# Kernel optimization log

Hardware: AMD Instinct MI355X
Metric: run time of the kernel (lower is better)

Reference implementation:

```python
import jax, jax.numpy as jnp
import numpy as np

N = 100000      # nodes
E = 1600000     # edges (avg degree 16)
IN_F, HID, OUT_F, NC = 384, 128, 64, 2
EPS = 1e-5
NEG_SLOPE = 0.01


def _layernorm(x, g, b):
    m = jnp.mean(x, axis=-1, keepdims=True)
    v = jnp.var(x, axis=-1, keepdims=True)
    return (x - m) * jax.lax.rsqrt(v + EPS) * g + b


def _graph_conv(x, edge_index, edge_weight, w_rel, b_rel, w_root):
    # PyG GraphConv: lin_rel(scatter_add(w_e * x[src] -> dst)) + lin_root(x)
    src, dst = edge_index[0], edge_index[1]
    msg = x[src] * edge_weight[:, None]                      # [E, C]
    agg = jax.ops.segment_sum(msg, dst, num_segments=x.shape[0])  # [N, C]
    return agg @ w_rel.T + b_rel + x @ w_root.T


def _xavier(key, shape):
    fan_in, fan_out = shape[1], shape[0]
    lim = float(np.sqrt(6.0 / (fan_in + fan_out)))
    return jax.random.uniform(key, shape, jnp.float32, -lim, lim)


def setup_inputs() -> dict:
    key = jax.random.key(0)
    ks = jax.random.split(key, 10)
    x = jax.random.normal(ks[0], (N, IN_F), jnp.float32)
    edge_index = jax.random.randint(ks[1], (2, E), 0, N, jnp.int64)
    edge_attr = jax.random.uniform(ks[2], (E,), jnp.float32)
    return {
        "x": x,
        "edge_index": edge_index,
        "edge_attr": edge_attr,
        "ln1_g": jnp.ones((IN_F,), jnp.float32),
        "ln1_b": jnp.zeros((IN_F,), jnp.float32),
        "fc1_w": _xavier(ks[3], (HID, IN_F)),
        "fc1_b": jnp.zeros((HID,), jnp.float32),
        "c1_wrel": _xavier(ks[4], (HID, HID)),
        "c1_brel": jnp.zeros((HID,), jnp.float32),
        "c1_wroot": _xavier(ks[5], (HID, HID)),
        "c2_wrel": _xavier(ks[6], (OUT_F, HID)),
        "c2_brel": jnp.zeros((OUT_F,), jnp.float32),
        "c2_wroot": _xavier(ks[7], (OUT_F, HID)),
        "ln2_g": jnp.ones((OUT_F,), jnp.float32),
        "ln2_b": jnp.zeros((OUT_F,), jnp.float32),
        "fc2_w": _xavier(ks[8], (NC, OUT_F)),
        "fc2_b": jnp.zeros((NC,), jnp.float32),
    }


def reference(x, edge_index, edge_attr,
              ln1_g, ln1_b, fc1_w, fc1_b,
              c1_wrel, c1_brel, c1_wroot,
              c2_wrel, c2_brel, c2_wroot,
              ln2_g, ln2_b, fc2_w, fc2_b):
    h = _layernorm(x, ln1_g, ln1_b) @ fc1_w.T + fc1_b          # [N, HID]
    h = _graph_conv(h, edge_index, edge_attr, c1_wrel, c1_brel, c1_wroot)
    h = jax.nn.leaky_relu(h, NEG_SLOPE)
    h = _graph_conv(h, edge_index, edge_attr, c2_wrel, c2_brel, c2_wroot)
    h = jax.nn.leaky_relu(h, NEG_SLOPE)                        # [N, OUT_F]
    out = _layernorm(h, ln2_g, ln2_b) @ fc2_w.T + fc2_b        # [N, NC]
    return out
```

## Files before the change

kernel.cpp:

```cpp
#include <hip/hip_runtime.h>
#include <hip/hip_bf16.h>

#define N_IN_F 384
#define N_HID  128
#define N_OUT  64

typedef unsigned short ushort_t;
typedef __attribute__((ext_vector_type(8))) short short8v;
typedef __attribute__((ext_vector_type(4))) float floatx4;

union U8 { uint4 v; unsigned short u[8]; };

__device__ __forceinline__ float bfu2f(unsigned short s){
    union { unsigned i; float f; } c; c.i = ((unsigned)s) << 16; return c.f;
}
__device__ __forceinline__ unsigned short f2bfu(float f){
    __hip_bfloat16 h = __float2bfloat16(f);
    union { __hip_bfloat16 h; unsigned short u; } c; c.h = h; return c.u;
}

__device__ __forceinline__ float loadS(const void* p, size_t i, int fm){
    return fm ? bfu2f(((const unsigned short*)p)[i]) : ((const float*)p)[i];
}

__global__ void k_detect_all(const int* __restrict__ ei, const unsigned* __restrict__ xw,
                             int* __restrict__ modep){
    int lane = threadIdx.x & 63;
    int zi = 0;
    if (lane < 32) zi = ei[2*lane + 1];
    int cnt = 0;
    #pragma unroll
    for (int q = 0; q < 8; q++){
        unsigned w = xw[lane*8 + q];
        unsigned elo = (w >> 7) & 0xff;
        cnt += (elo >= 118 && elo <= 134) ? 1 : 0;
    }
    #pragma unroll
    for (int m = 32; m; m >>= 1){ zi |= __shfl_xor(zi, m, 64); cnt += __shfl_xor(cnt, m, 64); }
    if (lane == 0 && blockIdx.x == 0){
        modep[0] = (zi == 0) ? 1 : 0;
        modep[1] = (cnt >= 256) ? 1 : 0;
    }
}

__device__ __forceinline__ int edge_src(const int* ei, int e, int i, int mode){
    return mode ? ei[2*(size_t)i] : ei[i];
}
__device__ __forceinline__ int edge_dst(const int* ei, int e, int i, int mode){
    return mode ? ei[2*(size_t)e + 2*(size_t)i] : ei[(size_t)e + i];
}

__global__ void k_hist(const int* __restrict__ ei, int e, int n, const int* __restrict__ modep,
                       int* __restrict__ deg, unsigned* __restrict__ rel){
    int i = blockIdx.x * 256 + threadIdx.x;
    if (i >= e) return;
    int mode = modep[0];
    int d = edge_dst(ei, e, i, mode);
    if ((unsigned)d >= (unsigned)n) return;
    rel[i] = (unsigned)atomicAdd(&deg[d], 1);
}

__global__ __launch_bounds__(1024) void k_blksum(
    const int* __restrict__ deg, int n, int* __restrict__ part)
{
    __shared__ int s[1024];
    int i = blockIdx.x * 1024 + threadIdx.x;
    s[threadIdx.x] = (i < n) ? deg[i] : 0;
    __syncthreads();
    for (int off = 512; off; off >>= 1){
        if (threadIdx.x < off) s[threadIdx.x] += s[threadIdx.x + off];
        __syncthreads();
    }
    if (threadIdx.x == 0) part[blockIdx.x] = s[0];
}

__global__ __launch_bounds__(128) void k_scanpart(
    int* __restrict__ part, int nb, int* __restrict__ rowoff, int n)
{
    __shared__ int s[128];
    int t = threadIdx.x;
    if (nb <= 128){
        int v = (t < nb) ? part[t] : 0;
        s[t] = v; __syncthreads();
        #pragma unroll
        for (int off = 1; off < 128; off <<= 1){
            int tmp = (t >= off) ? s[t - off] : 0;
            __syncthreads();
            s[t] += tmp;
            __syncthreads();
        }
        if (t < nb) part[t] = s[t] - v;
        if (t == 127) rowoff[n] = s[127];
    } else if (t == 0){
        int run = 0;
        for (int b = 0; b < nb; b++){ int tt = part[b]; part[b] = run; run += tt; }
        rowoff[n] = run;
    }
}

__global__ __launch_bounds__(1024) void k_scanblk(
    int* __restrict__ deg, const int* __restrict__ part, int n, int* __restrict__ rowoff)
{
    __shared__ int s[1024];
    int t = threadIdx.x;
    int i = blockIdx.x * 1024 + t;
    int v = (i < n) ? deg[i] : 0;
    s[t] = v; __syncthreads();
    for (int off = 1; off < 1024; off <<= 1){
        int tmp = (t >= off) ? s[t - off] : 0;
        __syncthreads();
        s[t] += tmp;
        __syncthreads();
    }
    if (i < n){
        int excl = s[t] - v + part[blockIdx.x];
        rowoff[i] = excl;
        deg[i]    = excl;
    }
}

__global__ void k_scatter(const int* __restrict__ ei, const void* __restrict__ ea,
                          int e, int n, const int* __restrict__ modep,
                          int* __restrict__ cursor, int2* __restrict__ colw)
{
    int i = blockIdx.x * 256 + threadIdx.x;
    if (i >= e) return;
    int mode = modep[0], fm = modep[1];
    int d = edge_dst(ei, e, i, mode);
    if ((unsigned)d >= (unsigned)n) return;
    int s = edge_src(ei, e, i, mode);
    if ((unsigned)s >= (unsigned)n) s = 0;
    int pos = atomicAdd(&cursor[d], 1);
    if ((unsigned)pos >= (unsigned)e) return;
    int2 pk; pk.x = s; pk.y = __float_as_int(loadS(ea, i, fm));
    colw[pos] = pk;
}

#define SC_CHUNK 2048
#define SC_BSHIFT 13
#define SC_MAXB 1024
__global__ __launch_bounds__(256) void k_scoarse(
    const int* __restrict__ ei, const void* __restrict__ ea,
    const unsigned* __restrict__ rel, const int* __restrict__ rowoff,
    const int* __restrict__ modep, int e, int n, int B,
    int4* __restrict__ tmp, int* __restrict__ off2)
{
    __shared__ int  hcnt[SC_MAXB];
    __shared__ int  hoff[SC_MAXB + 1];
    __shared__ int4 stage[SC_CHUNK];
    int t = threadIdx.x;
    int c = blockIdx.x;
    int chunk0 = c * SC_CHUNK;
    int mode = modep[0], fm = modep[1];

    for (int q = t; q < B; q += 256) hcnt[q] = 0;
    __syncthreads();

    int  pos[8], sv[8], wv[8];
    bool val[8];
    #pragma unroll
    for (int k = 0; k < 8; k++){
        int i = chunk0 + k*256 + t;
        val[k] = false;
        if (i < e){
            int d = edge_dst(ei, e, i, mode);
            if ((unsigned)d < (unsigned)n){
                int s = edge_src(ei, e, i, mode);
                if ((unsigned)s >= (unsigned)n) s = 0;
                int p = rowoff[d] + (int)rel[i];
                pos[k] = p; sv[k] = s; wv[k] = __float_as_int(loadS(ea, i, fm));
                val[k] = true;
                atomicAdd(&hcnt[p >> SC_BSHIFT], 1);
            }
        }
    }
    __syncthreads();
    if (t == 0){
        int run = 0;
        for (int q = 0; q < B; q++){ hoff[q] = run; run += hcnt[q]; }
        hoff[B] = run;
    }
    __syncthreads();
    for (int q = t; q < B; q += 256) hcnt[q] = 0;
    for (int q = t; q <= B; q += 256) off2[(size_t)c*(B+1) + q] = hoff[q];
    __syncthreads();
    #pragma unroll
    for (int k = 0; k < 8; k++){
        if (val[k]){
            int b = pos[k] >> SC_BSHIFT;
            int slot = hoff[b] + atomicAdd(&hcnt[b], 1);
            stage[slot] = make_int4(pos[k], sv[k], wv[k], 0);
        }
    }
    __syncthreads();
    int tot = hoff[B];
    for (int idx = t; idx < tot; idx += 256)
        tmp[(size_t)chunk0 + idx] = stage[idx];
}

__global__ __launch_bounds__(512) void k_sfine(
    const int4* __restrict__ tmp, const int* __restrict__ off2,
    int B, int nchunks, int2* __restrict__ colw)
{
    int b = blockIdx.x;
    int wv = threadIdx.x >> 6, lane = threadIdx.x & 63;
    const int NW = 8;
    int c = wv;
    if (c >= nchunks) return;
    int s0 = off2[(size_t)c*(B+1) + b];
    int s1 = off2[(size_t)c*(B+1) + b + 1];
    while (true){
        int cn = c + NW;
        int n0 = 0, n1 = 0;
        if (cn < nchunks){
            n0 = off2[(size_t)cn*(B+1) + b];
            n1 = off2[(size_t)cn*(B+1) + b + 1];
        }
        int len = s1 - s0;
        size_t base = (size_t)c * SC_CHUNK + s0;
        for (int k = lane; k < len; k += 64){
            int4 ent = tmp[base + k];
            colw[ent.x] = make_int2(ent.y, ent.z);
        }
        if (cn >= nchunks) break;
        c = cn; s0 = n0; s1 = n1;
    }
}

__global__ __launch_bounds__(64) void k_prep_w1(
    const void* __restrict__ W, const void* __restrict__ g, const void* __restrict__ b,
    const void* __restrict__ fc1b, const int* __restrict__ fmp,
    ushort_t* __restrict__ Wp, float* __restrict__ u, float* __restrict__ v)
{
    int fm = fmp[0];
    int j = blockIdx.x, lane = threadIdx.x;
    int ni = j >> 4, r16 = j & 15;
    float su = 0.f, sv = 0.f;
    for (int k = lane; k < N_IN_F; k += 64){
        float w  = loadS(W, (size_t)j*N_IN_F + k, fm);
        float gk = loadS(g, k, fm);
        float bk = loadS(b, k, fm);
        unsigned short pw = f2bfu(gk * w);
        int idx = ((((k >> 5)*8 + ni)*64) + (((k >> 3) & 3) << 4) + r16)*8 + (k & 7);
        Wp[idx] = pw;
        su += bfu2f(pw);
        sv += bk * w;
    }
    #pragma unroll
    for (int m = 32; m; m >>= 1){ su += __shfl_xor(su, m, 64); sv += __shfl_xor(sv, m, 64); }
    if (lane == 0){
        u[j] = su;
        v[j] = sv + loadS(fc1b, j, fm);
    }
}

__global__ void k_cvt4(const void* __restrict__ p0, const void* __restrict__ p1,
                       const void* __restrict__ p2, const void* __restrict__ p3,
                       const int* __restrict__ fmp, ushort_t* __restrict__ o)
{
    int fm = fmp[0];
    int i = blockIdx.x * 256 + threadIdx.x;
    if (i >= 49152) return;
    const void* p; int off, base, NI;
    if (i < 16384)      { p = p0; off = i;         base = 0;     NI = 8; }
    else if (i < 32768) { p = p1; off = i - 16384; base = 16384; NI = 8; }
    else if (i < 40960) { p = p2; off = i - 32768; base = 32768; NI = 4; }
    else                { p = p3; off = i - 40960; base = 40960; NI = 4; }
    int j = off >> 7, k = off & 127;
    int fidx = ((((k >> 5)*NI + (j >> 4))*64) + (((k >> 3) & 3) << 4) + (j & 15))*8 + (k & 7);
    o[base + fidx] = f2bfu(loadS(p, off, fm));
}

__global__ __launch_bounds__(512) void k_gemm1_mfma(
    const void* __restrict__ x, const int* __restrict__ fmp,
    const ushort_t* __restrict__ Wp,
    const float* __restrict__ u, const float* __restrict__ v,
    ushort_t* __restrict__ out, int n)
{
    __shared__ ushort_t Bs[24576];
    int fm = fmp[0];
    int t = threadIdx.x;
    int wave = t >> 6, lane = t & 63;
    int r16 = lane & 15, kq = lane >> 4;
    int m0 = blockIdx.x * 128;
    int mw = m0 + wave * 16;
    int grow = min(mw + r16, n - 1);

    const ushort_t* xbf = (const ushort_t*)x + (size_t)grow*N_IN_F + kq*8;
    const float*    xf  = (const float*)x    + (size_t)grow*N_IN_F + kq*8;

    floatx4 acc[8];
    #pragma unroll
    for (int c = 0; c < 8; c++) acc[c] = (floatx4){0.f,0.f,0.f,0.f};
    float s1 = 0.f, s2 = 0.f;

    #pragma unroll
    for (int h = 0; h < 2; h++){
        if (h) __syncthreads();
        {
            const uint4* src = (const uint4*)(Wp + h*24576);
            uint4* dst = (uint4*)Bs;
            #pragma unroll
            for (int q = 0; q < 12; q++) dst[t + q*512] = src[t + q*512];
        }
        __syncthreads();
        #pragma unroll
        for (int ksl = 0; ksl < 6; ksl++){
            int ks = h*6 + ksl;
            short8v af;
            if (fm){
                af = *(const short8v*)(xbf + ks*32);
            } else {
                floatx4 p  = *(const floatx4*)(xf + ks*32);
                floatx4 q4 = *(const floatx4*)(xf + ks*32 + 4);
                union { ushort_t u[8]; short8v v; } w_;
                w_.u[0]=f2bfu(p[0]);  w_.u[1]=f2bfu(p[1]);  w_.u[2]=f2bfu(p[2]);  w_.u[3]=f2bfu(p[3]);
                w_.u[4]=f2bfu(q4[0]); w_.u[5]=f2bfu(q4[1]); w_.u[6]=f2bfu(q4[2]); w_.u[7]=f2bfu(q4[3]);
                af = w_.v;
            }
            #pragma unroll
            for (int q = 0; q < 8; q++){
                float f = bfu2f((unsigned short)af[q]);
                s1 += f; s2 += f*f;
            }
            #pragma unroll
            for (int ni = 0; ni < 8; ni++){
                short8v bf = *(const short8v*)(Bs + ((ksl*8 + ni)*64 + lane)*8);
                acc[ni] = __builtin_amdgcn_mfma_f32_16x16x32_bf16(af, bf, acc[ni], 0, 0, 0);
            }
        }
    }

    s1 += __shfl_xor(s1, 16, 64); s1 += __shfl_xor(s1, 32, 64);
    s2 += __shfl_xor(s2, 16, 64); s2 += __shfl_xor(s2, 32, 64);
    float mu = s1 * (1.f/384.f);
    float var = fmaxf(s2 * (1.f/384.f) - mu*mu, 0.f);
    float rs = rsqrtf(var + 1e-5f);

    float mm[4], rr[4];
    #pragma unroll
    for (int r = 0; r < 4; r++){
        mm[r] = __shfl(mu, kq*4 + r, 64);
        rr[r] = __shfl(rs, kq*4 + r, 64);
    }
    int ib = mw + kq*4;
    #pragma unroll
    for (int ni = 0; ni < 8; ni++){
        int j = ni*16 + r16;
        float uj = u[j], vj = v[j];
        #pragma unroll
        for (int r = 0; r < 4; r++){
            int ii = ib + r;
            float val = rr[r]*acc[ni][r] - rr[r]*mm[r]*uj + vj;
            if (ii < n) out[(size_t)ii*N_HID + j] = f2bfu(val);
        }
    }
}

__global__ __launch_bounds__(512) void k_conv1_mfma(
    const ushort_t* __restrict__ A1, const ushort_t* __restrict__ A2,
    const ushort_t* __restrict__ W1f, const ushort_t* __restrict__ W2f,
    const void* __restrict__ bias, const int* __restrict__ fmp,
    ushort_t* __restrict__ out, int n)
{
    __shared__ ushort_t Bs[16384];
    int fm = fmp[0];
    int t = threadIdx.x;
    int wave = t >> 6, lane = t & 63;
    int r16 = lane & 15, kq = lane >> 4;
    int m0 = blockIdx.x * 128;
    int mw = m0 + wave * 16;
    int grow = min(mw + r16, n - 1);
    size_t aoff = (size_t)grow*N_HID + kq*8;

    floatx4 acc[8];
    #pragma unroll
    for (int c = 0; c < 8; c++) acc[c] = (floatx4){0.f,0.f,0.f,0.f};

    #pragma unroll
    for (int h = 0; h < 2; h++){
        if (h) __syncthreads();
        {
            const uint4* src = (const uint4*)(h ? W2f : W1f);
            uint4* dst = (uint4*)Bs;
            #pragma unroll
            for (int q = 0; q < 8; q++) dst[t + q*512] = src[t + q*512];
        }
        __syncthreads();
        const ushort_t* Asrc = h ? A2 : A1;
        #pragma unroll
        for (int ksl = 0; ksl < 4; ksl++){
            short8v af = *(const short8v*)(Asrc + aoff + ksl*32);
            #pragma unroll
            for (int ni = 0; ni < 8; ni++){
                short8v bf = *(const short8v*)(Bs + ((ksl*8 + ni)*64 + lane)*8);
                acc[ni] = __builtin_amdgcn_mfma_f32_16x16x32_bf16(af, bf, acc[ni], 0, 0, 0);
            }
        }
    }

    int ib = mw + kq*4;
    #pragma unroll
    for (int ni = 0; ni < 8; ni++){
        int j = ni*16 + r16;
        float bb = loadS(bias, j, fm);
        #pragma unroll
        for (int r = 0; r < 4; r++){
            int ii = ib + r;
            float val = acc[ni][r] + bb;
            val = (val >= 0.f) ? val : 0.01f * val;
            if (ii < n) out[(size_t)ii*N_HID + j] = f2bfu(val);
        }
    }
}

__global__ __launch_bounds__(512) void k_conv2_final(
    const ushort_t* __restrict__ A1, const ushort_t* __restrict__ A2,
    const ushort_t* __restrict__ Wall,
    const void* __restrict__ bias,
    const void* __restrict__ gam, const void* __restrict__ bet,
    const void* __restrict__ Wfc, const void* __restrict__ bfc,
    const int* __restrict__ fmp, void* __restrict__ out, int n)
{
    __shared__ ushort_t Bs[16384];
    int fm = fmp[0];
    int t = threadIdx.x;
    int wave = t >> 6, lane = t & 63;
    int r16 = lane & 15, kq = lane >> 4;
    int m0 = blockIdx.x * 128;
    int mw = m0 + wave * 16;
    int grow = min(mw + r16, n - 1);
    size_t aoff = (size_t)grow*N_HID + kq*8;

    {
        const uint4* src = (const uint4*)Wall;
        uint4* dst = (uint4*)Bs;
        #pragma unroll
        for (int q = 0; q < 8; q++) dst[t + q*512] = src[t + q*512];
    }
    __syncthreads();

    floatx4 acc[4];
    #pragma unroll
    for (int c = 0; c < 4; c++) acc[c] = (floatx4){0.f,0.f,0.f,0.f};

    #pragma unroll
    for (int ks = 0; ks < 8; ks++){
        const ushort_t* Asrc = (ks < 4) ? A1 : A2;
        short8v af = *(const short8v*)(Asrc + aoff + (ks & 3)*32);
        int cbase = (ks < 4) ? 0 : 16;
        #pragma unroll
        for (int ni = 0; ni < 4; ni++){
            int chunk = cbase + (ks & 3)*4 + ni;
            short8v bf = *(const short8v*)(Bs + (chunk*64 + lane)*8);
            acc[ni] = __builtin_amdgcn_mfma_f32_16x16x32_bf16(af, bf, acc[ni], 0, 0, 0);
        }
    }

    float b0 = loadS(bfc, 0, fm), b1 = loadS(bfc, 1, fm);
    float s[4] = {}, s2[4] = {};
    #pragma unroll
    for (int ni = 0; ni < 4; ni++){
        int j = ni*16 + r16;
        float bb = loadS(bias, j, fm);
        #pragma unroll
        for (int r = 0; r < 4; r++){
            float val = acc[ni][r] + bb;
            val = (val >= 0.f) ? val : 0.01f * val;
            acc[ni][r] = val;
            s[r] += val; s2[r] += val*val;
        }
    }
    #pragma unroll
    for (int m = 1; m < 16; m <<= 1){
        #pragma unroll
        for (int r = 0; r < 4; r++){
            s[r]  += __shfl_xor(s[r],  m, 64);
            s2[r] += __shfl_xor(s2[r], m, 64);
        }
    }
    float mu[4], rstd[4];
    #pragma unroll
    for (int r = 0; r < 4; r++){
        mu[r] = s[r] * (1.f/64.f);
        float var = fmaxf(s2[r] * (1.f/64.f) - mu[r]*mu[r], 0.f);
        rstd[r] = rsqrtf(var + 1e-5f);
    }
    float p0[4] = {}, p1[4] = {};
    #pragma unroll
    for (int ni = 0; ni < 4; ni++){
        int j = ni*16 + r16;
        float gj = loadS(gam, j, fm), bj = loadS(bet, j, fm);
        float w0 = loadS(Wfc, j, fm), w1 = loadS(Wfc, 64 + j, fm);
        #pragma unroll
        for (int r = 0; r < 4; r++){
            float zn = (acc[ni][r] - mu[r]) * rstd[r] * gj + bj;
            p0[r] += zn * w0;
            p1[r] += zn * w1;
        }
    }
    #pragma unroll
    for (int m = 1; m < 16; m <<= 1){
        #pragma unroll
        for (int r = 0; r < 4; r++){
            p0[r] += __shfl_xor(p0[r], m, 64);
            p1[r] += __shfl_xor(p1[r], m, 64);
        }
    }
    if (r16 == 0){
        #pragma unroll
        for (int r = 0; r < 4; r++){
            int ii = mw + kq*4 + r;
            if (ii >= n) continue;
            float o0 = p0[r] + b0, o1 = p1[r] + b1;
            if (fm){
                unsigned pk = ((unsigned)f2bfu(o1) << 16) | (unsigned)f2bfu(o0);
                *(unsigned*)((ushort_t*)out + (size_t)ii*2) = pk;
            } else {
                float2 f2; f2.x = o0; f2.y = o1;
                *(float2*)((float*)out + (size_t)ii*2) = f2;
            }
        }
    }
}

__global__ __launch_bounds__(256) void k_agg(
    const int* __restrict__ rowoff, const int2* __restrict__ colw,
    const ushort_t* __restrict__ src_mat,
    ushort_t* __restrict__ out, int n, int eTot)
{
    int t = threadIdx.x;
    int lane = t & 63;
    int d = blockIdx.x * 4 + (t >> 6);
    if (d >= n) return;
    int grp = lane >> 4;
    int c16 = lane & 15;
    int e0 = rowoff[d], e1 = rowoff[d+1];
    e0 = max(0, min(e0, eTot));
    e1 = max(e0, min(e1, eTot));
    float acc[8] = {};
    for (int e = e0 + grp; e < e1; e += 4){
        int2 cw = colw[e];
        int s = cw.x;
        if ((unsigned)s >= (unsigned)n) s = 0;
        float wv = __int_as_float(cw.y);
        U8 u; u.v = *(const uint4*)(src_mat + (size_t)s*N_HID + c16*8);
        #pragma unroll
        for (int q = 0; q < 8; q++) acc[q] += wv * bfu2f(u.u[q]);
    }
    #pragma unroll
    for (int q = 0; q < 8; q++){
        acc[q] += __shfl_xor(acc[q], 16, 64);
        acc[q] += __shfl_xor(acc[q], 32, 64);
    }
    if (grp == 0){
        union { ushort_t u[8]; uint4 v; } P;
        #pragma unroll
        for (int q = 0; q < 8; q++) P.u[q] = f2bfu(acc[q]);
        *(uint4*)(out + (size_t)d*N_HID + c16*8) = P.v;
    }
}

extern "C" void kernel_launch(void* const* d_in, const int* in_sizes, int n_in,
                              void* d_out, int out_size, void* d_ws, size_t ws_size,
                              hipStream_t stream)
{
    const void* x     = d_in[0];
    const int*  ei    = (const int*)d_in[1];
    const void* ea    = d_in[2];
    const void* ln1g  = d_in[3];
    const void* ln1b  = d_in[4];
    const void* fc1w  = d_in[5];
    const void* fc1b  = d_in[6];
    const void* c1rel = d_in[7];
    const void* c1bre = d_in[8];
    const void* c1roo = d_in[9];
    const void* c2rel = d_in[10];
    const void* c2bre = d_in[11];
    const void* c2roo = d_in[12];
    const void* ln2g  = d_in[13];
    const void* ln2b  = d_in[14];
    const void* fc2w  = d_in[15];
    const void* fc2b  = d_in[16];
    (void)n_in; (void)out_size; (void)ws_size;

    const int n = in_sizes[0] / N_IN_F;
    const int e = in_sizes[2];

    const int nchunks = (e + SC_CHUNK - 1) / SC_CHUNK;
    const int B = (e + (1 << SC_BSHIFT) - 1) >> SC_BSHIFT;

    char* wsp = (char*)d_ws;
    size_t off = 0;
    auto alloc = [&](size_t bytes) -> char* {
        char* p = wsp + off; off += (bytes + 255) & ~(size_t)255; return p;
    };
    int*      deg    = (int*)  alloc((size_t)n * 4);
    int*      rowoff = (int*)  alloc((size_t)(n+1) * 4);
    int*      part   = (int*)  alloc(4096);
    int*      modep  = (int*)  alloc(256);
    int2*     colw   = (int2*) alloc((size_t)e * 8);
    unsigned* rel    = (unsigned*)alloc((size_t)e * 4);
    int4*     stmp   = (int4*) alloc((size_t)e * 16);
    int*      off2   = (int*)  alloc((size_t)nchunks * (B+1) * 4);
    float*    u      = (float*)alloc(128 * 4);
    float*    v      = (float*)alloc(128 * 4);
    ushort_t* Wp     = (ushort_t*)alloc((size_t)N_HID * N_IN_F * 2);
    ushort_t* cw     = (ushort_t*)alloc((size_t)49152 * 2);
    ushort_t* h1     = (ushort_t*)alloc((size_t)n * N_HID * 2);
    ushort_t* agg1   = (ushort_t*)alloc((size_t)n * N_HID * 2);
    ushort_t* g1     = (ushort_t*)alloc((size_t)n * N_HID * 2);
    ushort_t* agg2   = h1;

    hipMemsetAsync(deg, 0, (size_t)n * 4, stream);
    k_detect_all<<<1, 64, 0, stream>>>(ei, (const unsigned*)x, modep);

    int nb = (n + 1023) / 1024;
    k_hist    <<<(e + 255) / 256, 256, 0, stream>>>(ei, e, n, modep, deg, rel);
    k_blksum  <<<nb, 1024, 0, stream>>>(deg, n, part);
    k_scanpart<<<1, 128, 0, stream>>>(part, nb, rowoff, n);
    k_scanblk <<<nb, 1024, 0, stream>>>(deg, part, n, rowoff);

    if (B <= SC_MAXB){
        k_scoarse<<<nchunks, 256, 0, stream>>>(ei, ea, rel, rowoff, modep, e, n, B, stmp, off2);
        k_sfine  <<<B, 512, 0, stream>>>(stmp, off2, B, nchunks, colw);
    } else {
        k_scatter<<<(e + 255) / 256, 256, 0, stream>>>(ei, ea, e, n, modep, deg, colw);
    }

    k_prep_w1<<<N_HID, 64, 0, stream>>>(fc1w, ln1g, ln1b, fc1b, modep + 1, Wp, u, v);
    k_cvt4   <<<(49152 + 255) / 256, 256, 0, stream>>>(c1rel, c1roo, c2rel, c2roo, modep + 1, cw);

    k_gemm1_mfma<<<(n + 127) / 128, 512, 0, stream>>>(x, modep + 1, Wp, u, v, h1, n);

    k_agg<<<(n + 3) / 4, 256, 0, stream>>>(rowoff, colw, h1, agg1, n, e);
    k_conv1_mfma<<<(n + 127) / 128, 512, 0, stream>>>(agg1, h1, cw, cw + 16384, c1bre, modep + 1, g1, n);

    k_agg<<<(n + 3) / 4, 256, 0, stream>>>(rowoff, colw, g1, agg2, n, e);
    k_conv2_final<<<(n + 127) / 128, 512, 0, stream>>>(agg2, g1, cw + 32768, c2bre,
                                                       ln2g, ln2b, fc2w, fc2b, modep + 1, d_out, n);
}
```

Before: 628.3 us.

## Fuse neighbor aggregation into GraphConv MFMA kernels via LDS fragments

Removes the standalone k_agg kernels. Each 128-row GEMM block now gathers the weighted neighbor sums for its rows directly into LDS, laid out in MFMA A-fragment order, and consumes them from there. This avoids writing and re-reading the aggregated N×128 bf16 intermediates and drops two launches. In exchange, the gather is serialized per wave over 16 rows, LDS use per block doubles to 64KB (which lowers occupancy), and the latency-bound gather has less parallelism to hide memory stalls.

```diff
diff --git a/kernel.cpp b/kernel.cpp
--- a/kernel.cpp
+++ b/kernel.cpp
@@ -357,12 +357,52 @@
     }
 }
 
-__global__ __launch_bounds__(512) void k_conv1_mfma(
-    const ushort_t* __restrict__ A1, const ushort_t* __restrict__ A2,
+__device__ __forceinline__ void gather_rows_to_frags(
+    ushort_t* Al, const int* rowoff, const int2* colw,
+    const ushort_t* src_mat, int n, int eTot,
+    int wave, int lane, int m0)
+{
+    int grp = lane >> 4;
+    int c16 = lane & 15;
+    for (int dr = 0; dr < 16; dr++){
+        int d = m0 + wave*16 + dr;
+        float acc[8] = {};
+        if (d < n){
+            int e0 = rowoff[d], e1 = rowoff[d+1];
+            e0 = max(0, min(e0, eTot));
+            e1 = max(e0, min(e1, eTot));
+            for (int e = e0 + grp; e < e1; e += 4){
+                int2 cw = colw[e];
+                int s = cw.x;
+                if ((unsigned)s >= (unsigned)n) s = 0;
+                float wv = __int_as_float(cw.y);
+                U8 u; u.v = *(const uint4*)(src_mat + (size_t)s*N_HID + c16*8);
+                #pragma unroll
+                for (int q = 0; q < 8; q++) acc[q] += wv * bfu2f(u.u[q]);
+            }
+        }
+        #pragma unroll
+        for (int q = 0; q < 8; q++){
+            acc[q] += __shfl_xor(acc[q], 16, 64);
+            acc[q] += __shfl_xor(acc[q], 32, 64);
+        }
+        if (grp == 0){
+            union { ushort_t u[8]; uint4 v; } P;
+            #pragma unroll
+            for (int q = 0; q < 8; q++) P.u[q] = f2bfu(acc[q]);
+            *(uint4*)(Al + (((wave*4 + (c16 >> 2))*64) + ((c16 & 3) << 4) + dr)*8) = P.v;
+        }
+    }
+}
+
+__global__ __launch_bounds__(512) void k_conv1_fused(
+    const int* __restrict__ rowoff, const int2* __restrict__ colw,
+    const ushort_t* __restrict__ H,
     const ushort_t* __restrict__ W1f, const ushort_t* __restrict__ W2f,
     const void* __restrict__ bias, const int* __restrict__ fmp,
-    ushort_t* __restrict__ out, int n)
-{
+    ushort_t* __restrict__ out, int n, int eTot)
+{
+    __shared__ ushort_t Al[16384];
     __shared__ ushort_t Bs[16384];
     int fm = fmp[0];
     int t = threadIdx.x;
@@ -373,29 +413,43 @@
     int grow = min(mw + r16, n - 1);
     size_t aoff = (size_t)grow*N_HID + kq*8;
 
+    gather_rows_to_frags(Al, rowoff, colw, H, n, eTot, wave, lane, m0);
+
     floatx4 acc[8];
     #pragma unroll
     for (int c = 0; c < 8; c++) acc[c] = (floatx4){0.f,0.f,0.f,0.f};
 
-    #pragma unroll
-    for (int h = 0; h < 2; h++){
-        if (h) __syncthreads();
-        {
-            const uint4* src = (const uint4*)(h ? W2f : W1f);
-            uint4* dst = (uint4*)Bs;
-            #pragma unroll
-            for (int q = 0; q < 8; q++) dst[t + q*512] = src[t + q*512];
-        }
-        __syncthreads();
-        const ushort_t* Asrc = h ? A2 : A1;
-        #pragma unroll
-        for (int ksl = 0; ksl < 4; ksl++){
-            short8v af = *(const short8v*)(Asrc + aoff + ksl*32);
-            #pragma unroll
-            for (int ni = 0; ni < 8; ni++){
-                short8v bf = *(const short8v*)(Bs + ((ksl*8 + ni)*64 + lane)*8);
-                acc[ni] = __builtin_amdgcn_mfma_f32_16x16x32_bf16(af, bf, acc[ni], 0, 0, 0);
-            }
+    {
+        const uint4* src = (const uint4*)W1f;
+        uint4* dst = (uint4*)Bs;
+        #pragma unroll
+        for (int q = 0; q < 8; q++) dst[t + q*512] = src[t + q*512];
+    }
+    __syncthreads();
+    #pragma unroll
+    for (int ksl = 0; ksl < 4; ksl++){
+        short8v af = *(const short8v*)(Al + ((wave*4 + ksl)*64 + lane)*8);
+        #pragma unroll
+        for (int ni = 0; ni < 8; ni++){
+            short8v bf = *(const short8v*)(Bs + ((ksl*8 + ni)*64 + lane)*8);
+            acc[ni] = __builtin_amdgcn_mfma_f32_16x16x32_bf16(af, bf, acc[ni], 0, 0, 0);
+        }
+    }
+    __syncthreads();
+    {
+        const uint4* src = (const uint4*)W2f;
+        uint4* dst = (uint4*)Bs;
+        #pragma unroll
+        for (int q = 0; q < 8; q++) dst[t + q*512] = src[t + q*512];
+    }
+    __syncthreads();
+    #pragma unroll
+    for (int ksl = 0; ksl < 4; ksl++){
+        short8v af = *(const short8v*)(H + aoff + ksl*32);
+        #pragma unroll
+        for (int ni = 0; ni < 8; ni++){
+            short8v bf = *(const short8v*)(Bs + ((ksl*8 + ni)*64 + lane)*8);
+            acc[ni] = __builtin_amdgcn_mfma_f32_16x16x32_bf16(af, bf, acc[ni], 0, 0, 0);
         }
     }
 
@@ -414,14 +468,16 @@
     }
 }
 
-__global__ __launch_bounds__(512) void k_conv2_final(
-    const ushort_t* __restrict__ A1, const ushort_t* __restrict__ A2,
+__global__ __launch_bounds__(512) void k_conv2_fused(
+    const int* __restrict__ rowoff, const int2* __restrict__ colw,
+    const ushort_t* __restrict__ G,
     const ushort_t* __restrict__ Wall,
     const void* __restrict__ bias,
     const void* __restrict__ gam, const void* __restrict__ bet,
     const void* __restrict__ Wfc, const void* __restrict__ bfc,
-    const int* __restrict__ fmp, void* __restrict__ out, int n)
-{
+    const int* __restrict__ fmp, void* __restrict__ out, int n, int eTot)
+{
+    __shared__ ushort_t Al[16384];
     __shared__ ushort_t Bs[16384];
     int fm = fmp[0];
     int t = threadIdx.x;
@@ -438,6 +494,7 @@
         #pragma unroll
         for (int q = 0; q < 8; q++) dst[t + q*512] = src[t + q*512];
     }
+    gather_rows_to_frags(Al, rowoff, colw, G, n, eTot, wave, lane, m0);
     __syncthreads();
 
     floatx4 acc[4];
@@ -446,8 +503,9 @@
 
     #pragma unroll
     for (int ks = 0; ks < 8; ks++){
-        const ushort_t* Asrc = (ks < 4) ? A1 : A2;
-        short8v af = *(const short8v*)(Asrc + aoff + (ks & 3)*32);
+        short8v af;
+        if (ks < 4) af = *(const short8v*)(Al + ((wave*4 + ks)*64 + lane)*8);
+        else        af = *(const short8v*)(G + aoff + (ks & 3)*32);
         int cbase = (ks < 4) ? 0 : 16;
         #pragma unroll
         for (int ni = 0; ni < 4; ni++){
@@ -521,43 +579,6 @@
                 *(float2*)((float*)out + (size_t)ii*2) = f2;
             }
         }
-    }
-}
-
-__global__ __launch_bounds__(256) void k_agg(
-    const int* __restrict__ rowoff, const int2* __restrict__ colw,
-    const ushort_t* __restrict__ src_mat,
-    ushort_t* __restrict__ out, int n, int eTot)
-{
-    int t = threadIdx.x;
-    int lane = t & 63;
-    int d = blockIdx.x * 4 + (t >> 6);
-    if (d >= n) return;
-    int grp = lane >> 4;
-    int c16 = lane & 15;
-    int e0 = rowoff[d], e1 = rowoff[d+1];
-    e0 = max(0, min(e0, eTot));
-    e1 = max(e0, min(e1, eTot));
-    float acc[8] = {};
-    for (int e = e0 + grp; e < e1; e += 4){
-        int2 cw = colw[e];
-        int s = cw.x;
-        if ((unsigned)s >= (unsigned)n) s = 0;
-        float wv = __int_as_float(cw.y);
-        U8 u; u.v = *(const uint4*)(src_mat + (size_t)s*N_HID + c16*8);
-        #pragma unroll
-        for (int q = 0; q < 8; q++) acc[q] += wv * bfu2f(u.u[q]);
-    }
-    #pragma unroll
-    for (int q = 0; q < 8; q++){
-        acc[q] += __shfl_xor(acc[q], 16, 64);
-        acc[q] += __shfl_xor(acc[q], 32, 64);
-    }
-    if (grp == 0){
-        union { ushort_t u[8]; uint4 v; } P;
-        #pragma unroll
-        for (int q = 0; q < 8; q++) P.u[q] = f2bfu(acc[q]);
-        *(uint4*)(out + (size_t)d*N_HID + c16*8) = P.v;
     }
 }
 
@@ -608,9 +629,7 @@
     ushort_t* Wp     = (ushort_t*)alloc((size_t)N_HID * N_IN_F * 2);
     ushort_t* cw     = (ushort_t*)alloc((size_t)49152 * 2);
     ushort_t* h1     = (ushort_t*)alloc((size_t)n * N_HID * 2);
-    ushort_t* agg1   = (ushort_t*)alloc((size_t)n * N_HID * 2);
     ushort_t* g1     = (ushort_t*)alloc((size_t)n * N_HID * 2);
-    ushort_t* agg2   = h1;
 
     hipMemsetAsync(deg, 0, (size_t)n * 4, stream);
     k_detect_all<<<1, 64, 0, stream>>>(ei, (const unsigned*)x, modep);
@@ -633,10 +652,10 @@
 
     k_gemm1_mfma<<<(n + 127) / 128, 512, 0, stream>>>(x, modep + 1, Wp, u, v, h1, n);
 
-    k_agg<<<(n + 3) / 4, 256, 0, stream>>>(rowoff, colw, h1, agg1, n, e);
-    k_conv1_mfma<<<(n + 127) / 128, 512, 0, stream>>>(agg1, h1, cw, cw + 16384, c1bre, modep + 1, g1, n);
-
-    k_agg<<<(n + 3) / 4, 256, 0, stream>>>(rowoff, colw, g1, agg2, n, e);
-    k_conv2_final<<<(n + 127) / 128, 512, 0, stream>>>(agg2, g1, cw + 32768, c2bre,
-                                                       ln2g, ln2b, fc2w, fc2b, modep + 1, d_out, n);
-}
+    k_conv1_fused<<<(n + 127) / 128, 512, 0, stream>>>(rowoff, colw, h1, cw, cw + 16384,
+                                                       c1bre, modep + 1, g1, n, e);
+
+    k_conv2_fused<<<(n + 127) / 128, 512, 0, stream>>>(rowoff, colw, g1, cw + 32768, c2bre,
+                                                       ln2g, ln2b, fc2w, fc2b, modep + 1,
+                                                       d_out, n, e);
+}
```

New measurement: 728.1 us. 1.16x slower.
